# Kernel optimization log

Hardware: AMD Instinct MI355X
Metric: run time of the kernel (lower is better)

## Reference

```python
import jax, jax.numpy as jnp
import numpy as np

M_DIM = 1024
N_HEADS = 16
H_DIM = M_DIM // N_HEADS
FFN_H = 2 * M_DIM
B, S = 2, 2048
EPS = 1e-5
NEG = -1e9


def layernorm(x, g, b):
    mu = jnp.mean(x, axis=-1, keepdims=True)
    var = jnp.mean((x - mu) ** 2, axis=-1, keepdims=True)
    return (x - mu) * jax.lax.rsqrt(var + EPS) * g + b


def setup_inputs() -> dict:
    key = jax.random.key(0)
    ks = jax.random.split(key, 16)
    sc = 0.02
    return {
        "x": jax.random.normal(ks[0], (B, S, M_DIM), jnp.float32),
        "attention_mask": jnp.ones((B, S), jnp.int32),
        # per-head QKV projections stacked over heads: [H, M, D]
        "Wq": jax.random.normal(ks[1], (N_HEADS, M_DIM, H_DIM), jnp.float32) * sc,
        "bq": jnp.zeros((N_HEADS, H_DIM), jnp.float32),
        "Wk": jax.random.normal(ks[2], (N_HEADS, M_DIM, H_DIM), jnp.float32) * sc,
        "bk": jnp.zeros((N_HEADS, H_DIM), jnp.float32),
        "Wv": jax.random.normal(ks[3], (N_HEADS, M_DIM, H_DIM), jnp.float32) * sc,
        "bv": jnp.zeros((N_HEADS, H_DIM), jnp.float32),
        "Wo": jax.random.normal(ks[4], (M_DIM, M_DIM), jnp.float32) * sc,
        "bo": jnp.zeros((M_DIM,), jnp.float32),
        "g1": jnp.ones((M_DIM,), jnp.float32),
        "b1": jnp.zeros((M_DIM,), jnp.float32),
        "W1": jax.random.normal(ks[5], (M_DIM, FFN_H), jnp.float32) * sc,
        "bias1": jnp.zeros((FFN_H,), jnp.float32),
        "W2": jax.random.normal(ks[6], (FFN_H, M_DIM), jnp.float32) * sc,
        "bias2": jnp.zeros((M_DIM,), jnp.float32),
        "g2": jnp.ones((M_DIM,), jnp.float32),
        "b2": jnp.zeros((M_DIM,), jnp.float32),
    }


def reference(x, attention_mask, Wq, bq, Wk, bk, Wv, bv, Wo, bo, g1, b1, W1, bias1, W2, bias2, g2, b2):
    # All heads at once (the torch code loops over heads; same math).
    q = jnp.einsum("bsm,hmd->bhsd", x, Wq) + bq[None, :, None, :]
    k = jnp.einsum("bsm,hmd->bhsd", x, Wk) + bk[None, :, None, :]
    v = jnp.einsum("bsm,hmd->bhsd", x, Wv) + bv[None, :, None, :]
    scores = jnp.einsum("bhqd,bhkd->bhqk", q, k) / jnp.sqrt(jnp.float32(H_DIM))
    mask = attention_mask[:, None, None, :].astype(bool)  # [B,1,1,S] over keys
    scores = jnp.where(mask, scores, NEG)
    attn = jax.nn.softmax(scores, axis=-1)
    ctx = jnp.einsum("bhqk,bhkd->bhqd", attn, v)
    ctx = ctx.transpose(0, 2, 1, 3).reshape(x.shape[0], x.shape[1], M_DIM)  # concat heads
    out = ctx @ Wo + bo
    out = layernorm(out + x, g1, b1)
    fout = jax.nn.relu(out @ W1 + bias1) @ W2 + bias2
    out = layernorm(out + fout, g2, b2)
    return out
```

## Files before the change

### kernel.cpp

```cpp
#include <hip/hip_runtime.h>

#define MDIM 1024
#define FFH  2048
#define SEQ  2048
#define AST  72
#define VST  136
#define QSCL 0.18033688f

#if __has_builtin(__builtin_amdgcn_exp2f)
  #define EXP2(x) __builtin_amdgcn_exp2f(x)
#else
  #define EXP2(x) exp2f(x)
#endif

typedef __attribute__((ext_vector_type(8))) __bf16 bf16x8;
typedef __attribute__((ext_vector_type(4))) float floatx4;
typedef __attribute__((ext_vector_type(8))) unsigned short ushort8;
typedef __attribute__((address_space(3))) unsigned int lds_uint;
typedef const __attribute__((address_space(1))) unsigned int g_uint;

__device__ __forceinline__ unsigned short f2bf(float f){
  union { float f; unsigned u; } v; v.f = f;
  unsigned u = v.u;
  u += 0x7fffu + ((u >> 16) & 1u);
  return (unsigned short)(u >> 16);
}
__device__ __forceinline__ unsigned short f2bf_tr(float f){
  union { float f; unsigned u; } v; v.f = f;
  return (unsigned short)(v.u >> 16);
}

__global__ void k_cvt_qb(const float* __restrict__ x, unsigned short* __restrict__ xb,
                         const float* __restrict__ bq, const float* __restrict__ bk,
                         const float* __restrict__ bv, float* __restrict__ qbias){
  const int bid = blockIdx.x, t = threadIdx.x;
  if (bid < 4096){
    int i = (bid * 256 + t) * 4;
    float4 v = *(const float4*)(x + i);
    ushort4 o;
    o.x = f2bf(v.x); o.y = f2bf(v.y); o.z = f2bf(v.z); o.w = f2bf(v.w);
    *(ushort4*)(xb + i) = o;
  } else {
    int i = (bid - 4096) * 256 + t;
    qbias[i] = (i < 1024) ? bq[i] * QSCL : (i < 2048) ? bk[i - 1024] : bv[i - 2048];
  }
}

__global__ void __launch_bounds__(256) k_prep_w(const float* __restrict__ Wo, const float* __restrict__ W1,
                                                const float* __restrict__ W2, const float* __restrict__ Wq,
                                                const float* __restrict__ Wk, const float* __restrict__ Wv,
                                                unsigned short* __restrict__ wot, unsigned short* __restrict__ w1t,
                                                unsigned short* __restrict__ w2t, unsigned short* __restrict__ wqkvt){
  __shared__ unsigned short Ts[32 * 36];
  const int t = threadIdx.x, bid = blockIdx.x;
  const int lr = t >> 3, lc4 = (t & 7) << 2;
  if (bid >= 5120){
    const int id = bid - 5120;
    const int xm = id & 31, yd = (id >> 5) & 1, z = id >> 6;
    const int tensor = z >> 4, h = z & 15;
    const float* W = (tensor == 0) ? Wq : (tensor == 1) ? Wk : Wv;
    const float scl = (tensor == 0) ? QSCL : 1.0f;
    const int m0 = xm << 5, d0 = yd << 5;
    float4 v = *(const float4*)(W + ((size_t)h << 16) + (size_t)(m0 + lr) * 64 + d0 + lc4);
    ushort4 o; o.x = f2bf(v.x * scl); o.y = f2bf(v.y * scl); o.z = f2bf(v.z * scl); o.w = f2bf(v.w * scl);
    *(ushort4*)&Ts[lr * 36 + lc4] = o;
    __syncthreads();
    ushort4 w;
    w.x = Ts[(lc4 + 0) * 36 + lr];
    w.y = Ts[(lc4 + 1) * 36 + lr];
    w.z = Ts[(lc4 + 2) * 36 + lr];
    w.w = Ts[(lc4 + 3) * 36 + lr];
    const int n = (tensor << 10) + (h << 6) + d0 + lr;
    *(ushort4*)(wqkvt + ((size_t)n << 10) + m0 + lc4) = w;
    return;
  }
  const float* src; unsigned short* dst; int K, N, k0, n0;
  if (bid < 1024){
    src = Wo; dst = wot; K = 1024; N = 1024;
    n0 = (bid & 31) << 5; k0 = (bid >> 5) << 5;
  } else if (bid < 3072){
    const int id = bid - 1024;
    src = W1; dst = w1t; K = 1024; N = 2048;
    n0 = (id & 63) << 5; k0 = (id >> 6) << 5;
  } else {
    const int id = bid - 3072;
    src = W2; dst = w2t; K = 2048; N = 1024;
    n0 = (id & 31) << 5; k0 = (id >> 5) << 5;
  }
  float4 v = *(const float4*)(src + (size_t)(k0 + lr) * N + n0 + lc4);
  ushort4 o; o.x = f2bf(v.x); o.y = f2bf(v.y); o.z = f2bf(v.z); o.w = f2bf(v.w);
  *(ushort4*)&Ts[lr * 36 + lc4] = o;
  __syncthreads();
  ushort4 w;
  w.x = Ts[(lc4 + 0) * 36 + lr];
  w.y = Ts[(lc4 + 1) * 36 + lr];
  w.z = Ts[(lc4 + 2) * 36 + lr];
  w.w = Ts[(lc4 + 3) * 36 + lr];
  *(ushort4*)(dst + (size_t)(n0 + lr) * K + k0 + lc4) = w;
}

template<int RELU, int OUTBF>
__global__ void __launch_bounds__(256, 3) k_gemm128(const unsigned short* __restrict__ A,
                                                 const unsigned short* __restrict__ Bt,
                                                 const float* __restrict__ bias,
                                                 void* __restrict__ Cout, int N, int K){
  __shared__ unsigned short As[2][128 * 32];
  __shared__ unsigned short Bs[2][128 * 32];
  const int t = threadIdx.x;
  const int m0 = blockIdx.y << 7, n0 = blockIdx.x << 7;
  const int lane = t & 63, w = t >> 6;
  const int quad = lane >> 4, l16 = lane & 15;
  const int mw = (w & 1) << 6, nw = (w >> 1) << 6;
  floatx4 acc[4][4];
  #pragma unroll
  for (int i = 0; i < 4; i++)
    #pragma unroll
    for (int j = 0; j < 4; j++) acc[i][j] = (floatx4){0.f, 0.f, 0.f, 0.f};
  const unsigned short* Ag  = A  + (size_t)(m0 + (t >> 2)) * K + ((t & 3) << 3);
  const unsigned short* Ag2 = Ag + (size_t)64 * K;
  const unsigned short* Bg  = Bt + (size_t)(n0 + (t >> 2)) * K + ((t & 3) << 3);
  const unsigned short* Bg2 = Bg + (size_t)64 * K;

#define STG128(Ad, Bd, kb) { \
    __builtin_amdgcn_global_load_lds((g_uint*)(Ag  + (kb)), (lds_uint*)&(Ad)[t << 3],          16, 0, 0); \
    __builtin_amdgcn_global_load_lds((g_uint*)(Ag2 + (kb)), (lds_uint*)&(Ad)[(t << 3) + 2048], 16, 0, 0); \
    __builtin_amdgcn_global_load_lds((g_uint*)(Bg  + (kb)), (lds_uint*)&(Bd)[t << 3],          16, 0, 0); \
    __builtin_amdgcn_global_load_lds((g_uint*)(Bg2 + (kb)), (lds_uint*)&(Bd)[(t << 3) + 2048], 16, 0, 0); \
  }

  STG128(As[0], Bs[0], 0);
  __syncthreads();
  int cur = 0;
  for (int kb = 0; kb < K; kb += 32){
    if (kb + 32 < K) STG128(As[cur ^ 1], Bs[cur ^ 1], kb + 32);
    const unsigned short* Ar = As[cur];
    const unsigned short* Br = Bs[cur];
    bf16x8 af[4], bf[4];
    #pragma unroll
    for (int mt = 0; mt < 4; mt++)
      af[mt] = *(const bf16x8*)&Ar[((mw + (mt << 4) + l16) << 5) + (quad << 3)];
    #pragma unroll
    for (int nt = 0; nt < 4; nt++)
      bf[nt] = *(const bf16x8*)&Br[((nw + (nt << 4) + l16) << 5) + (quad << 3)];
    #pragma unroll
    for (int mt = 0; mt < 4; mt++)
      #pragma unroll
      for (int nt = 0; nt < 4; nt++)
        acc[mt][nt] = __builtin_amdgcn_mfma_f32_16x16x32_bf16(af[mt], bf[nt], acc[mt][nt], 0, 0, 0);
    __syncthreads();
    cur ^= 1;
  }
#undef STG128
  #pragma unroll
  for (int nt = 0; nt < 4; nt++){
    const int col = n0 + nw + (nt << 4) + l16;
    const float bsv = bias[col];
    #pragma unroll
    for (int mt = 0; mt < 4; mt++){
      const int row = m0 + mw + (mt << 4) + (quad << 2);
      #pragma unroll
      for (int r = 0; r < 4; r++){
        float v = acc[mt][nt][r] + bsv;
        if (RELU) v = fmaxf(v, 0.f);
        if (OUTBF) ((unsigned short*)Cout)[(size_t)(row + r) * N + col] = f2bf(v);
        else       ((float*)Cout)[(size_t)(row + r) * N + col] = v;
      }
    }
  }
}

template<int RELU, int OUTBF>
__global__ void __launch_bounds__(256) k_gemm64n(const unsigned short* __restrict__ A,
                                                 const unsigned short* __restrict__ Bt,
                                                 const float* __restrict__ bias,
                                                 void* __restrict__ Cout, int N, int K){
  __shared__ unsigned short As[2][2 * 128 * 32];
  __shared__ unsigned short Bs[2][2 * 64 * 32];
  const int t = threadIdx.x;
  const int m0 = blockIdx.y << 7, n0 = blockIdx.x << 6;
  const int lane = t & 63, w = t >> 6;
  const int quad = lane >> 4, l16 = lane & 15;
  const int mw = (w & 1) << 6, nw = (w >> 1) << 5;
  floatx4 acc[4][2];
  #pragma unroll
  for (int i = 0; i < 4; i++)
    #pragma unroll
    for (int j = 0; j < 2; j++) acc[i][j] = (floatx4){0.f, 0.f, 0.f, 0.f};
  const unsigned short* Ag  = A  + (size_t)(m0 + (t >> 2)) * K + ((t & 3) << 3);
  const unsigned short* Ag2 = Ag + (size_t)64 * K;
  const unsigned short* Bg  = Bt + (size_t)(n0 + (t >> 2)) * K + ((t & 3) << 3);

#define STG64(Ad, Bd, kb) { \
    _Pragma("unroll") \
    for (int s = 0; s < 2; s++){ \
      const int ko = (kb) + (s << 5); \
      __builtin_amdgcn_global_load_lds((g_uint*)(Ag  + ko), (lds_uint*)&(Ad)[(s << 12) + (t << 3)],        16, 0, 0); \
      __builtin_amdgcn_global_load_lds((g_uint*)(Ag2 + ko), (lds_uint*)&(Ad)[(s << 12) + (t << 3) + 2048], 16, 0, 0); \
      __builtin_amdgcn_global_load_lds((g_uint*)(Bg  + ko), (lds_uint*)&(Bd)[(s << 11) + (t << 3)],        16, 0, 0); \
    } }

  STG64(As[0], Bs[0], 0);
  __syncthreads();
  int cur = 0;
  for (int kb = 0; kb < K; kb += 64){
    if (kb + 64 < K) STG64(As[cur ^ 1], Bs[cur ^ 1], kb + 64);
    const unsigned short* Ar = As[cur];
    const unsigned short* Br = Bs[cur];
    #pragma unroll
    for (int s = 0; s < 2; s++){
      bf16x8 af[4], bf[2];
      #pragma unroll
      for (int mt = 0; mt < 4; mt++)
        af[mt] = *(const bf16x8*)&Ar[(s << 12) + ((mw + (mt << 4) + l16) << 5) + (quad << 3)];
      #pragma unroll
      for (int nt = 0; nt < 2; nt++)
        bf[nt] = *(const bf16x8*)&Br[(s << 11) + ((nw + (nt << 4) + l16) << 5) + (quad << 3)];
      #pragma unroll
      for (int mt = 0; mt < 4; mt++)
        #pragma unroll
        for (int nt = 0; nt < 2; nt++)
          acc[mt][nt] = __builtin_amdgcn_mfma_f32_16x16x32_bf16(af[mt], bf[nt], acc[mt][nt], 0, 0, 0);
    }
    __syncthreads();
    cur ^= 1;
  }
#undef STG64
  #pragma unroll
  for (int nt = 0; nt < 2; nt++){
    const int col = n0 + nw + (nt << 4) + l16;
    const float bsv = bias[col];
    #pragma unroll
    for (int mt = 0; mt < 4; mt++){
      const int row = m0 + mw + (mt << 4) + (quad << 2);
      #pragma unroll
      for (int r = 0; r < 4; r++){
        float v = acc[mt][nt][r] + bsv;
        if (RELU) v = fmaxf(v, 0.f);
        if (OUTBF) ((unsigned short*)Cout)[(size_t)(row + r) * N + col] = f2bf(v);
        else       ((float*)Cout)[(size_t)(row + r) * N + col] = v;
      }
    }
  }
}

__global__ void __launch_bounds__(256, 2) k_attn(const unsigned short* __restrict__ qkvb,
                                                 const int* __restrict__ amask,
                                                 unsigned short* __restrict__ ctxb){
  __shared__ __align__(16) unsigned short Ks[2][128 * AST];
  __shared__ __align__(16) unsigned short Vt[2][64 * VST];
  __shared__ __align__(16) int msk[2][128];
  const int t = threadIdx.x;
  const int w = t >> 6, lane = t & 63;
  const int quad = lane >> 4, l16 = lane & 15;
  const int lin = (blockIdx.y << 4) | blockIdx.x;
  const int xcd = lin & 7, jj = lin >> 3;
  const int bh = (xcd << 2) | (jj >> 4);
  const int b = bh >> 4, h = bh & 15;
  const int q0 = (jj & 15) << 7;
  const int r0 = (w << 5) + l16;
  const int r1 = r0 + 16;
  const int sr = t >> 2, sc = (t & 3) << 4;
  const int kg = t >> 4, dc = (t & 15) << 2;
  const int swz  = (dc >> 4) & 3;
  const int pc0  = ((((kg & 3) | ((kg >> 3) << 2)) ^ swz) << 3) | (((kg >> 2) & 1) << 2);

  {
    const int qr = t >> 1, qc = (t & 1) << 5;
    const unsigned short* qs = qkvb + (size_t)((b << 11) + q0 + qr) * 3072 + (h << 6) + qc;
    unsigned short* qd = &Ks[0][qr * AST + qc];
    *(uint4*)(qd)      = *(const uint4*)(qs);
    *(uint4*)(qd + 8)  = *(const uint4*)(qs + 8);
    *(uint4*)(qd + 16) = *(const uint4*)(qs + 16);
    *(uint4*)(qd + 24) = *(const uint4*)(qs + 24);
  }
  __syncthreads();
  const bf16x8 qa0 = *(const bf16x8*)&Ks[0][r0 * AST + (quad << 3)];
  const bf16x8 qa1 = *(const bf16x8*)&Ks[0][r0 * AST + (quad << 3) + 32];
  const bf16x8 qb0 = *(const bf16x8*)&Ks[0][r1 * AST + (quad << 3)];
  const bf16x8 qb1 = *(const bf16x8*)&Ks[0][r1 * AST + (quad << 3) + 32];

  floatx4 accA[4], accB[4];
  #pragma unroll
  for (int i = 0; i < 4; i++){
    accA[i] = (floatx4){0.f, 0.f, 0.f, 0.f};
    accB[i] = (floatx4){0.f, 0.f, 0.f, 0.f};
  }
  float l_runA = 0.f, l_runB = 0.f;

  const unsigned short* kbase  = qkvb + (size_t)((b << 11) + sr) * 3072 + 1024 + (h << 6) + sc;
  const unsigned short* kbase2 = kbase + (size_t)64 * 3072;
  const unsigned short* vbase  = qkvb + (size_t)((b << 11) + (kg << 2)) * 3072 + 2048 + (h << 6) + dc;
  const unsigned short* vbase2 = vbase + (size_t)64 * 3072;
  const int* mbase = amask + (b << 11);

  uint4 krA, krB, krC, krD;
  ushort4 va0, va1, va2, va3, vb0, vb1, vb2, vb3;
  int mreg = 1;

#define LOADT(tt) { \
    const size_t off = (size_t)((tt) << 7) * 3072; \
    krA = *(const uint4*)(kbase + off); \
    krB = *(const uint4*)(kbase + off + 8); \
    krC = *(const uint4*)(kbase2 + off); \
    krD = *(const uint4*)(kbase2 + off + 8); \
    va0 = *(const ushort4*)(vbase + off); \
    va1 = *(const ushort4*)(vbase + off + 3072); \
    va2 = *(const ushort4*)(vbase + off + 2 * 3072); \
    va3 = *(const ushort4*)(vbase + off + 3 * 3072); \
    vb0 = *(const ushort4*)(vbase2 + off); \
    vb1 = *(const ushort4*)(vbase2 + off + 3072); \
    vb2 = *(const ushort4*)(vbase2 + off + 2 * 3072); \
    vb3 = *(const ushort4*)(vbase2 + off + 3 * 3072); \
    if (t < 128) mreg = mbase[((tt) << 7) + t]; \
  }

#define STORET(dst) { \
    unsigned short* Kd = Ks[dst]; \
    unsigned short* Vd = Vt[dst]; \
    *(uint4*)&Kd[sr * AST + sc]            = krA; \
    *(uint4*)&Kd[sr * AST + sc + 8]        = krB; \
    *(uint4*)&Kd[(sr + 64) * AST + sc]     = krC; \
    *(uint4*)&Kd[(sr + 64) * AST + sc + 8] = krD; \
    ushort4 cc; \
    cc.x = va0.x; cc.y = va1.x; cc.z = va2.x; cc.w = va3.x; *(ushort4*)&Vd[(dc + 0) * VST + pc0] = cc; \
    cc.x = va0.y; cc.y = va1.y; cc.z = va2.y; cc.w = va3.y; *(ushort4*)&Vd[(dc + 1) * VST + pc0] = cc; \
    cc.x = va0.z; cc.y = va1.z; cc.z = va2.z; cc.w = va3.z; *(ushort4*)&Vd[(dc + 2) * VST + pc0] = cc; \
    cc.x = va0.w; cc.y = va1.w; cc.z = va2.w; cc.w = va3.w; *(ushort4*)&Vd[(dc + 3) * VST + pc0] = cc; \
    cc.x = vb0.x; cc.y = vb1.x; cc.z = vb2.x; cc.w = vb3.x; *(ushort4*)&Vd[(dc + 0) * VST + pc0 + 64] = cc; \
    cc.x = vb0.y; cc.y = vb1.y; cc.z = vb2.y; cc.w = vb3.y; *(ushort4*)&Vd[(dc + 1) * VST + pc0 + 64] = cc; \
    cc.x = vb0.z; cc.y = vb1.z; cc.z = vb2.z; cc.w = vb3.z; *(ushort4*)&Vd[(dc + 2) * VST + pc0 + 64] = cc; \
    cc.x = vb0.w; cc.y = vb1.w; cc.z = vb2.w; cc.w = vb3.w; *(ushort4*)&Vd[(dc + 3) * VST + pc0 + 64] = cc; \
    if (t < 128) msk[dst][t] = mreg; \
  }

  LOADT(0);
  __syncthreads();
  STORET(0);
  LOADT(1);
  __syncthreads();

  int c = 0;
  for (int kt = 0; kt < 16; kt++){
    if (kt + 1 < 16) STORET(c ^ 1);
    if (kt + 2 < 16) LOADT(kt + 2);
    {
      const unsigned short* Kc = Ks[c];
      const unsigned short* Vc = Vt[c];
      const int* Mc = msk[c];
      float lsA = 0.f, lsB = 0.f;
      #pragma unroll
      for (int s = 0; s < 4; s++){
        const unsigned short* kp = &Kc[((s << 5) + l16) * AST + (quad << 3)];
        const bf16x8 k00 = *(const bf16x8*)(kp);
        const bf16x8 k01 = *(const bf16x8*)(kp + 32);
        const bf16x8 k10 = *(const bf16x8*)(kp + (AST << 4));
        const bf16x8 k11 = *(const bf16x8*)(kp + (AST << 4) + 32);
        floatx4 sA0 = (floatx4){0.f, 0.f, 0.f, 0.f};
        floatx4 sB0 = (floatx4){0.f, 0.f, 0.f, 0.f};
        floatx4 sA1 = (floatx4){0.f, 0.f, 0.f, 0.f};
        floatx4 sB1 = (floatx4){0.f, 0.f, 0.f, 0.f};
        __builtin_amdgcn_s_setprio(1);
        sA0 = __builtin_amdgcn_mfma_f32_16x16x32_bf16(k00, qa0, sA0, 0, 0, 0);
        sA0 = __builtin_amdgcn_mfma_f32_16x16x32_bf16(k01, qa1, sA0, 0, 0, 0);
        sB0 = __builtin_amdgcn_mfma_f32_16x16x32_bf16(k00, qb0, sB0, 0, 0, 0);
        sB0 = __builtin_amdgcn_mfma_f32_16x16x32_bf16(k01, qb1, sB0, 0, 0, 0);
        sA1 = __builtin_amdgcn_mfma_f32_16x16x32_bf16(k10, qa0, sA1, 0, 0, 0);
        sA1 = __builtin_amdgcn_mfma_f32_16x16x32_bf16(k11, qa1, sA1, 0, 0, 0);
        sB1 = __builtin_amdgcn_mfma_f32_16x16x32_bf16(k10, qb0, sB1, 0, 0, 0);
        sB1 = __builtin_amdgcn_mfma_f32_16x16x32_bf16(k11, qb1, sB1, 0, 0, 0);
        __builtin_amdgcn_s_setprio(0);
        const int4 m0 = *(const int4*)&Mc[(s << 5) + (quad << 2)];
        const int4 m1 = *(const int4*)&Mc[(s << 5) + 16 + (quad << 2)];
        const float a0 = m0.x ? EXP2(sA0[0]) : 0.f;
        const float a1 = m0.y ? EXP2(sA0[1]) : 0.f;
        const float a2 = m0.z ? EXP2(sA0[2]) : 0.f;
        const float a3 = m0.w ? EXP2(sA0[3]) : 0.f;
        const float a4 = m1.x ? EXP2(sA1[0]) : 0.f;
        const float a5 = m1.y ? EXP2(sA1[1]) : 0.f;
        const float a6 = m1.z ? EXP2(sA1[2]) : 0.f;
        const float a7 = m1.w ? EXP2(sA1[3]) : 0.f;
        const float b0 = m0.x ? EXP2(sB0[0]) : 0.f;
        const float b1 = m0.y ? EXP2(sB0[1]) : 0.f;
        const float b2 = m0.z ? EXP2(sB0[2]) : 0.f;
        const float b3 = m0.w ? EXP2(sB0[3]) : 0.f;
        const float b4 = m1.x ? EXP2(sB1[0]) : 0.f;
        const float b5 = m1.y ? EXP2(sB1[1]) : 0.f;
        const float b6 = m1.z ? EXP2(sB1[2]) : 0.f;
        const float b7 = m1.w ? EXP2(sB1[3]) : 0.f;
        lsA += (a0 + a1) + (a2 + a3) + (a4 + a5) + (a6 + a7);
        lsB += (b0 + b1) + (b2 + b3) + (b4 + b5) + (b6 + b7);
        ushort8 uA, uB;
        uA[0] = f2bf_tr(a0); uA[1] = f2bf_tr(a1); uA[2] = f2bf_tr(a2); uA[3] = f2bf_tr(a3);
        uA[4] = f2bf_tr(a4); uA[5] = f2bf_tr(a5); uA[6] = f2bf_tr(a6); uA[7] = f2bf_tr(a7);
        uB[0] = f2bf_tr(b0); uB[1] = f2bf_tr(b1); uB[2] = f2bf_tr(b2); uB[3] = f2bf_tr(b3);
        uB[4] = f2bf_tr(b4); uB[5] = f2bf_tr(b5); uB[6] = f2bf_tr(b6); uB[7] = f2bf_tr(b7);
        const bf16x8 pfA = __builtin_bit_cast(bf16x8, uA);
        const bf16x8 pfB = __builtin_bit_cast(bf16x8, uB);
        __builtin_amdgcn_s_setprio(1);
        #pragma unroll
        for (int mt = 0; mt < 4; mt++){
          const bf16x8 vf = *(const bf16x8*)&Vc[((mt << 4) + l16) * VST + ((((s << 2) + quad) ^ mt) << 3)];
          accA[mt] = __builtin_amdgcn_mfma_f32_16x16x32_bf16(vf, pfA, accA[mt], 0, 0, 0);
          accB[mt] = __builtin_amdgcn_mfma_f32_16x16x32_bf16(vf, pfB, accB[mt], 0, 0, 0);
        }
        __builtin_amdgcn_s_setprio(0);
      }
      l_runA += lsA;
      l_runB += lsB;
    }
    __syncthreads();
    c ^= 1;
  }
#undef LOADT
#undef STORET

  l_runA += __shfl_xor(l_runA, 16);
  l_runA += __shfl_xor(l_runA, 32);
  l_runB += __shfl_xor(l_runB, 16);
  l_runB += __shfl_xor(l_runB, 32);
  const float liA = 1.f / l_runA;
  const float liB = 1.f / l_runB;
  unsigned short* oA = ctxb + (size_t)((b << 11) + q0 + r0) * 1024 + (h << 6);
  unsigned short* oB = ctxb + (size_t)((b << 11) + q0 + r1) * 1024 + (h << 6);
  #pragma unroll
  for (int mt = 0; mt < 4; mt++){
    ushort4 o;
    o.x = f2bf(accA[mt][0] * liA);
    o.y = f2bf(accA[mt][1] * liA);
    o.z = f2bf(accA[mt][2] * liA);
    o.w = f2bf(accA[mt][3] * liA);
    *(ushort4*)&oA[(mt << 4) + (quad << 2)] = o;
    o.x = f2bf(accB[mt][0] * liB);
    o.y = f2bf(accB[mt][1] * liB);
    o.z = f2bf(accB[mt][2] * liB);
    o.w = f2bf(accB[mt][3] * liB);
    *(ushort4*)&oB[(mt << 4) + (quad << 2)] = o;
  }
}

__global__ void __launch_bounds__(256) k_ln(const unsigned short* __restrict__ a,
                                            const float* __restrict__ res,
                                            const float* __restrict__ gg, const float* __restrict__ bb,
                                            float* __restrict__ out, unsigned short* __restrict__ outb){
  const int row = blockIdx.x, t = threadIdx.x;
  const ushort4 au = ((const ushort4*)(a + (size_t)row * 1024))[t];
  const float4 rv = ((const float4*)(res + (size_t)row * 1024))[t];
  float4 v;
  { union { unsigned u; float f; } c;
    c.u = (unsigned)au.x << 16; v.x = c.f + rv.x;
    c.u = (unsigned)au.y << 16; v.y = c.f + rv.y;
    c.u = (unsigned)au.z << 16; v.z = c.f + rv.z;
    c.u = (unsigned)au.w << 16; v.w = c.f + rv.w; }
  float sum = v.x + v.y + v.z + v.w;
  float ss  = v.x * v.x + v.y * v.y + v.z * v.z + v.w * v.w;
  #pragma unroll
  for (int off = 32; off > 0; off >>= 1){
    sum += __shfl_down(sum, off);
    ss  += __shfl_down(ss, off);
  }
  __shared__ float red[8];
  const int w = t >> 6;
  if ((t & 63) == 0){ red[w] = sum; red[4 + w] = ss; }
  __syncthreads();
  const float S  = red[0] + red[1] + red[2] + red[3];
  const float SS = red[4] + red[5] + red[6] + red[7];
  const float mu  = S * (1.f / 1024.f);
  const float var = SS * (1.f / 1024.f) - mu * mu;
  const float rs  = rsqrtf(var + 1e-5f);
  const float4 gv = ((const float4*)gg)[t];
  const float4 bv = ((const float4*)bb)[t];
  float4 o;
  o.x = (v.x - mu) * rs * gv.x + bv.x;
  o.y = (v.y - mu) * rs * gv.y + bv.y;
  o.z = (v.z - mu) * rs * gv.z + bv.z;
  o.w = (v.w - mu) * rs * gv.w + bv.w;
  ((float4*)(out + (size_t)row * 1024))[t] = o;
  if (outb){
    ushort4 ob; ob.x = f2bf(o.x); ob.y = f2bf(o.y); ob.z = f2bf(o.z); ob.w = f2bf(o.w);
    ((ushort4*)(outb + (size_t)row * 1024))[t] = ob;
  }
}

extern "C" void kernel_launch(void* const* d_in, const int* in_sizes, int n_in,
                              void* d_out, int out_size, void* d_ws, size_t ws_size,
                              hipStream_t stream){
  const float* x     = (const float*)d_in[0];
  const int*   amask = (const int*)d_in[1];
  const float* Wq    = (const float*)d_in[2];
  const float* bq    = (const float*)d_in[3];
  const float* Wk    = (const float*)d_in[4];
  const float* bk    = (const float*)d_in[5];
  const float* Wv    = (const float*)d_in[6];
  const float* bv    = (const float*)d_in[7];
  const float* Wo    = (const float*)d_in[8];
  const float* bo    = (const float*)d_in[9];
  const float* g1    = (const float*)d_in[10];
  const float* b1    = (const float*)d_in[11];
  const float* W1    = (const float*)d_in[12];
  const float* bias1 = (const float*)d_in[13];
  const float* W2    = (const float*)d_in[14];
  const float* bias2 = (const float*)d_in[15];
  const float* g2    = (const float*)d_in[16];
  const float* b2    = (const float*)d_in[17];

  char* ws = (char*)d_ws;
  unsigned short* xb    = (unsigned short*)(ws + 0);
  unsigned short* wqkvt = (unsigned short*)(ws + 8388608);
  float*          qbias = (float*)         (ws + 14680064);
  unsigned short* wot   = (unsigned short*)(ws + 14692352);
  unsigned short* w1t   = (unsigned short*)(ws + 16789504);
  unsigned short* w2t   = (unsigned short*)(ws + 20983808);
  unsigned short* ctxb  = (unsigned short*)(ws + 25178112);
  unsigned short* attnb = (unsigned short*)(ws + 33566720);
  unsigned short* fbufb = attnb;
  unsigned short* qkvb  = (unsigned short*)(ws + 50343936);
  float*          out1  = (float*)         (ws + 50343936);
  unsigned short* out1b = (unsigned short*)(ws + 50343936 + 25165824);
  unsigned short* h1    = (unsigned short*)(ws + 50343936 + 33554432);

  k_cvt_qb<<<dim3(4108), dim3(256), 0, stream>>>(x, xb, bq, bk, bv, qbias);
  k_prep_w<<<dim3(8192), dim3(256), 0, stream>>>(Wo, W1, W2, Wq, Wk, Wv, wot, w1t, w2t, wqkvt);

  k_gemm128<0,1><<<dim3(24, 32), dim3(256), 0, stream>>>(xb, wqkvt, qbias, qkvb, 3072, 1024);
  k_attn<<<dim3(16, 32), dim3(256), 0, stream>>>(qkvb, amask, ctxb);
  k_gemm64n<0,1><<<dim3(16, 32), dim3(256), 0, stream>>>(ctxb, wot, bo, attnb, MDIM, 1024);
  k_ln<<<dim3(4096), dim3(256), 0, stream>>>(attnb, x, g1, b1, out1, out1b);
  k_gemm128<1,1><<<dim3(16, 32), dim3(256), 0, stream>>>(out1b, w1t, bias1, h1, FFH, 1024);
  k_gemm64n<0,1><<<dim3(16, 32), dim3(256), 0, stream>>>(h1, w2t, bias2, fbufb, MDIM, 2048);
  k_ln<<<dim3(4096), dim3(256), 0, stream>>>(fbufb, out1, g2, b2, (float*)d_out, nullptr);
}
```

Measured before the change: 297.2 us.

## Software-pipeline QK MFMAs one sub-tile ahead of softmax/PV in attention

Splits each 32-key sub-step of the attention inner loop into a QK^T MFMA stage and an exp/convert/PV stage, then interleaves them so the QK scores for sub-tile s+1 are issued before finishing sub-tile s. The aim is to hide MFMA latency behind the exp and conversion VALU work. It also drops the XCD-aware block index remapping in favour of a direct blockIdx mapping, which changes how heads spread over L2 domains. The extra live score registers may raise register pressure, which matters under launch_bounds(256,2).

```diff
diff --git a/kernel.cpp b/kernel.cpp
--- a/kernel.cpp
+++ b/kernel.cpp
@@ -252,11 +252,8 @@
   const int t = threadIdx.x;
   const int w = t >> 6, lane = t & 63;
   const int quad = lane >> 4, l16 = lane & 15;
-  const int lin = (blockIdx.y << 4) | blockIdx.x;
-  const int xcd = lin & 7, jj = lin >> 3;
-  const int bh = (xcd << 2) | (jj >> 4);
-  const int b = bh >> 4, h = bh & 15;
-  const int q0 = (jj & 15) << 7;
+  const int b = blockIdx.y >> 4, h = blockIdx.y & 15;
+  const int q0 = blockIdx.x << 7;
   const int r0 = (w << 5) + l16;
   const int r1 = r0 + 16;
   const int sr = t >> 2, sc = (t & 3) << 4;
@@ -333,6 +330,66 @@
     if (t < 128) msk[dst][t] = mreg; \
   }
 
+#define QKISS(s, SA0, SB0, SA1, SB1) { \
+    const unsigned short* kp = &Kc[(((s) << 5) + l16) * AST + (quad << 3)]; \
+    const bf16x8 k00 = *(const bf16x8*)(kp); \
+    const bf16x8 k01 = *(const bf16x8*)(kp + 32); \
+    const bf16x8 k10 = *(const bf16x8*)(kp + (AST << 4)); \
+    const bf16x8 k11 = *(const bf16x8*)(kp + (AST << 4) + 32); \
+    SA0 = (floatx4){0.f, 0.f, 0.f, 0.f}; \
+    SB0 = (floatx4){0.f, 0.f, 0.f, 0.f}; \
+    SA1 = (floatx4){0.f, 0.f, 0.f, 0.f}; \
+    SB1 = (floatx4){0.f, 0.f, 0.f, 0.f}; \
+    __builtin_amdgcn_s_setprio(1); \
+    SA0 = __builtin_amdgcn_mfma_f32_16x16x32_bf16(k00, qa0, SA0, 0, 0, 0); \
+    SA0 = __builtin_amdgcn_mfma_f32_16x16x32_bf16(k01, qa1, SA0, 0, 0, 0); \
+    SB0 = __builtin_amdgcn_mfma_f32_16x16x32_bf16(k00, qb0, SB0, 0, 0, 0); \
+    SB0 = __builtin_amdgcn_mfma_f32_16x16x32_bf16(k01, qb1, SB0, 0, 0, 0); \
+    SA1 = __builtin_amdgcn_mfma_f32_16x16x32_bf16(k10, qa0, SA1, 0, 0, 0); \
+    SA1 = __builtin_amdgcn_mfma_f32_16x16x32_bf16(k11, qa1, SA1, 0, 0, 0); \
+    SB1 = __builtin_amdgcn_mfma_f32_16x16x32_bf16(k10, qb0, SB1, 0, 0, 0); \
+    SB1 = __builtin_amdgcn_mfma_f32_16x16x32_bf16(k11, qb1, SB1, 0, 0, 0); \
+    __builtin_amdgcn_s_setprio(0); \
+  }
+
+#define FIN(s, SA0, SB0, SA1, SB1) { \
+    const int4 m0 = *(const int4*)&Mc[((s) << 5) + (quad << 2)]; \
+    const int4 m1 = *(const int4*)&Mc[((s) << 5) + 16 + (quad << 2)]; \
+    const float a0 = m0.x ? EXP2(SA0[0]) : 0.f; \
+    const float a1 = m0.y ? EXP2(SA0[1]) : 0.f; \
+    const float a2 = m0.z ? EXP2(SA0[2]) : 0.f; \
+    const float a3 = m0.w ? EXP2(SA0[3]) : 0.f; \
+    const float a4 = m1.x ? EXP2(SA1[0]) : 0.f; \
+    const float a5 = m1.y ? EXP2(SA1[1]) : 0.f; \
+    const float a6 = m1.z ? EXP2(SA1[2]) : 0.f; \
+    const float a7 = m1.w ? EXP2(SA1[3]) : 0.f; \
+    const float b0 = m0.x ? EXP2(SB0[0]) : 0.f; \
+    const float b1 = m0.y ? EXP2(SB0[1]) : 0.f; \
+    const float b2 = m0.z ? EXP2(SB0[2]) : 0.f; \
+    const float b3 = m0.w ? EXP2(SB0[3]) : 0.f; \
+    const float b4 = m1.x ? EXP2(SB1[0]) : 0.f; \
+    const float b5 = m1.y ? EXP2(SB1[1]) : 0.f; \
+    const float b6 = m1.z ? EXP2(SB1[2]) : 0.f; \
+    const float b7 = m1.w ? EXP2(SB1[3]) : 0.f; \
+    lsA += (a0 + a1) + (a2 + a3) + (a4 + a5) + (a6 + a7); \
+    lsB += (b0 + b1) + (b2 + b3) + (b4 + b5) + (b6 + b7); \
+    ushort8 uA, uB; \
+    uA[0] = f2bf_tr(a0); uA[1] = f2bf_tr(a1); uA[2] = f2bf_tr(a2); uA[3] = f2bf_tr(a3); \
+    uA[4] = f2bf_tr(a4); uA[5] = f2bf_tr(a5); uA[6] = f2bf_tr(a6); uA[7] = f2bf_tr(a7); \
+    uB[0] = f2bf_tr(b0); uB[1] = f2bf_tr(b1); uB[2] = f2bf_tr(b2); uB[3] = f2bf_tr(b3); \
+    uB[4] = f2bf_tr(b4); uB[5] = f2bf_tr(b5); uB[6] = f2bf_tr(b6); uB[7] = f2bf_tr(b7); \
+    const bf16x8 pfA = __builtin_bit_cast(bf16x8, uA); \
+    const bf16x8 pfB = __builtin_bit_cast(bf16x8, uB); \
+    __builtin_amdgcn_s_setprio(1); \
+    _Pragma("unroll") \
+    for (int mt = 0; mt < 4; mt++){ \
+      const bf16x8 vf = *(const bf16x8*)&Vc[((mt << 4) + l16) * VST + (((((s) << 2) + quad) ^ mt) << 3)]; \
+      accA[mt] = __builtin_amdgcn_mfma_f32_16x16x32_bf16(vf, pfA, accA[mt], 0, 0, 0); \
+      accB[mt] = __builtin_amdgcn_mfma_f32_16x16x32_bf16(vf, pfB, accB[mt], 0, 0, 0); \
+    } \
+    __builtin_amdgcn_s_setprio(0); \
+  }
+
   LOADT(0);
   __syncthreads();
   STORET(0);
@@ -348,63 +405,16 @@
       const unsigned short* Vc = Vt[c];
       const int* Mc = msk[c];
       float lsA = 0.f, lsB = 0.f;
-      #pragma unroll
-      for (int s = 0; s < 4; s++){
-        const unsigned short* kp = &Kc[((s << 5) + l16) * AST + (quad << 3)];
-        const bf16x8 k00 = *(const bf16x8*)(kp);
-        const bf16x8 k01 = *(const bf16x8*)(kp + 32);
-        const bf16x8 k10 = *(const bf16x8*)(kp + (AST << 4));
-        const bf16x8 k11 = *(const bf16x8*)(kp + (AST << 4) + 32);
-        floatx4 sA0 = (floatx4){0.f, 0.f, 0.f, 0.f};
-        floatx4 sB0 = (floatx4){0.f, 0.f, 0.f, 0.f};
-        floatx4 sA1 = (floatx4){0.f, 0.f, 0.f, 0.f};
-        floatx4 sB1 = (floatx4){0.f, 0.f, 0.f, 0.f};
-        __builtin_amdgcn_s_setprio(1);
-        sA0 = __builtin_amdgcn_mfma_f32_16x16x32_bf16(k00, qa0, sA0, 0, 0, 0);
-        sA0 = __builtin_amdgcn_mfma_f32_16x16x32_bf16(k01, qa1, sA0, 0, 0, 0);
-        sB0 = __builtin_amdgcn_mfma_f32_16x16x32_bf16(k00, qb0, sB0, 0, 0, 0);
-        sB0 = __builtin_amdgcn_mfma_f32_16x16x32_bf16(k01, qb1, sB0, 0, 0, 0);
-        sA1 = __builtin_amdgcn_mfma_f32_16x16x32_bf16(k10, qa0, sA1, 0, 0, 0);
-        sA1 = __builtin_amdgcn_mfma_f32_16x16x32_bf16(k11, qa1, sA1, 0, 0, 0);
-        sB1 = __builtin_amdgcn_mfma_f32_16x16x32_bf16(k10, qb0, sB1, 0, 0, 0);
-        sB1 = __builtin_amdgcn_mfma_f32_16x16x32_bf16(k11, qb1, sB1, 0, 0, 0);
-        __builtin_amdgcn_s_setprio(0);
-        const int4 m0 = *(const int4*)&Mc[(s << 5) + (quad << 2)];
-        const int4 m1 = *(const int4*)&Mc[(s << 5) + 16 + (quad << 2)];
-        const float a0 = m0.x ? EXP2(sA0[0]) : 0.f;
-        const float a1 = m0.y ? EXP2(sA0[1]) : 0.f;
-        const float a2 = m0.z ? EXP2(sA0[2]) : 0.f;
-        const float a3 = m0.w ? EXP2(sA0[3]) : 0.f;
-        const float a4 = m1.x ? EXP2(sA1[0]) : 0.f;
-        const float a5 = m1.y ? EXP2(sA1[1]) : 0.f;
-        const float a6 = m1.z ? EXP2(sA1[2]) : 0.f;
-        const float a7 = m1.w ? EXP2(sA1[3]) : 0.f;
-        const float b0 = m0.x ? EXP2(sB0[0]) : 0.f;
-        const float b1 = m0.y ? EXP2(sB0[1]) : 0.f;
-        const float b2 = m0.z ? EXP2(sB0[2]) : 0.f;
-        const float b3 = m0.w ? EXP2(sB0[3]) : 0.f;
-        const float b4 = m1.x ? EXP2(sB1[0]) : 0.f;
-        const float b5 = m1.y ? EXP2(sB1[1]) : 0.f;
-        const float b6 = m1.z ? EXP2(sB1[2]) : 0.f;
-        const float b7 = m1.w ? EXP2(sB1[3]) : 0.f;
-        lsA += (a0 + a1) + (a2 + a3) + (a4 + a5) + (a6 + a7);
-        lsB += (b0 + b1) + (b2 + b3) + (b4 + b5) + (b6 + b7);
-        ushort8 uA, uB;
-        uA[0] = f2bf_tr(a0); uA[1] = f2bf_tr(a1); uA[2] = f2bf_tr(a2); uA[3] = f2bf_tr(a3);
-        uA[4] = f2bf_tr(a4); uA[5] = f2bf_tr(a5); uA[6] = f2bf_tr(a6); uA[7] = f2bf_tr(a7);
-        uB[0] = f2bf_tr(b0); uB[1] = f2bf_tr(b1); uB[2] = f2bf_tr(b2); uB[3] = f2bf_tr(b3);
-        uB[4] = f2bf_tr(b4); uB[5] = f2bf_tr(b5); uB[6] = f2bf_tr(b6); uB[7] = f2bf_tr(b7);
-        const bf16x8 pfA = __builtin_bit_cast(bf16x8, uA);
-        const bf16x8 pfB = __builtin_bit_cast(bf16x8, uB);
-        __builtin_amdgcn_s_setprio(1);
-        #pragma unroll
-        for (int mt = 0; mt < 4; mt++){
-          const bf16x8 vf = *(const bf16x8*)&Vc[((mt << 4) + l16) * VST + ((((s << 2) + quad) ^ mt) << 3)];
-          accA[mt] = __builtin_amdgcn_mfma_f32_16x16x32_bf16(vf, pfA, accA[mt], 0, 0, 0);
-          accB[mt] = __builtin_amdgcn_mfma_f32_16x16x32_bf16(vf, pfB, accB[mt], 0, 0, 0);
-        }
-        __builtin_amdgcn_s_setprio(0);
-      }
+      floatx4 xA0, xB0, xA1, xB1;
+      floatx4 yA0, yB0, yA1, yB1;
+      QKISS(0, xA0, xB0, xA1, xB1);
+      QKISS(1, yA0, yB0, yA1, yB1);
+      FIN  (0, xA0, xB0, xA1, xB1);
+      QKISS(2, xA0, xB0, xA1, xB1);
+      FIN  (1, yA0, yB0, yA1, yB1);
+      QKISS(3, yA0, yB0, yA1, yB1);
+      FIN  (2, xA0, xB0, xA1, xB1);
+      FIN  (3, yA0, yB0, yA1, yB1);
       l_runA += lsA;
       l_runB += lsB;
     }
@@ -413,6 +423,8 @@
   }
 #undef LOADT
 #undef STORET
+#undef QKISS
+#undef FIN
 
   l_runA += __shfl_xor(l_runA, 16);
   l_runA += __shfl_xor(l_runA, 32);
```

New measurement: 302.2 us. No clear change (+1.7%).

## Single-buffer attention K/V tiles in LDS and raise occupancy to four blocks

Applied to the files above, without the earlier changes.

The attention kernel drops the double-buffered K/V/mask LDS tiles for a single buffer. Each iteration now stores the register-prefetched tile, syncs, then prefetches the next tile into registers while computing. Launch bounds go from 2 to 4 blocks per CU, and the XCD-aware block-index remapping is replaced by a plain blockIdx mapping. The aim is more resident waves to hide latency, at the cost of an extra barrier per tile, less LDS-level overlap, tighter register limits and possibly worse L2 locality across XCDs.

```diff
diff --git a/kernel.cpp b/kernel.cpp
--- a/kernel.cpp
+++ b/kernel.cpp
@@ -243,20 +243,17 @@
   }
 }
 
-__global__ void __launch_bounds__(256, 2) k_attn(const unsigned short* __restrict__ qkvb,
+__global__ void __launch_bounds__(256, 4) k_attn(const unsigned short* __restrict__ qkvb,
                                                  const int* __restrict__ amask,
                                                  unsigned short* __restrict__ ctxb){
-  __shared__ __align__(16) unsigned short Ks[2][128 * AST];
-  __shared__ __align__(16) unsigned short Vt[2][64 * VST];
-  __shared__ __align__(16) int msk[2][128];
+  __shared__ __align__(16) unsigned short Ks[128 * AST];
+  __shared__ __align__(16) unsigned short Vt[64 * VST];
+  __shared__ __align__(16) int msk[128];
   const int t = threadIdx.x;
   const int w = t >> 6, lane = t & 63;
   const int quad = lane >> 4, l16 = lane & 15;
-  const int lin = (blockIdx.y << 4) | blockIdx.x;
-  const int xcd = lin & 7, jj = lin >> 3;
-  const int bh = (xcd << 2) | (jj >> 4);
-  const int b = bh >> 4, h = bh & 15;
-  const int q0 = (jj & 15) << 7;
+  const int b = blockIdx.y >> 4, h = blockIdx.y & 15;
+  const int q0 = blockIdx.x << 7;
   const int r0 = (w << 5) + l16;
   const int r1 = r0 + 16;
   const int sr = t >> 2, sc = (t & 3) << 4;
@@ -267,17 +264,17 @@
   {
     const int qr = t >> 1, qc = (t & 1) << 5;
     const unsigned short* qs = qkvb + (size_t)((b << 11) + q0 + qr) * 3072 + (h << 6) + qc;
-    unsigned short* qd = &Ks[0][qr * AST + qc];
+    unsigned short* qd = &Ks[qr * AST + qc];
     *(uint4*)(qd)      = *(const uint4*)(qs);
     *(uint4*)(qd + 8)  = *(const uint4*)(qs + 8);
     *(uint4*)(qd + 16) = *(const uint4*)(qs + 16);
     *(uint4*)(qd + 24) = *(const uint4*)(qs + 24);
   }
   __syncthreads();
-  const bf16x8 qa0 = *(const bf16x8*)&Ks[0][r0 * AST + (quad << 3)];
-  const bf16x8 qa1 = *(const bf16x8*)&Ks[0][r0 * AST + (quad << 3) + 32];
-  const bf16x8 qb0 = *(const bf16x8*)&Ks[0][r1 * AST + (quad << 3)];
-  const bf16x8 qb1 = *(const bf16x8*)&Ks[0][r1 * AST + (quad << 3) + 32];
+  const bf16x8 qa0 = *(const bf16x8*)&Ks[r0 * AST + (quad << 3)];
+  const bf16x8 qa1 = *(const bf16x8*)&Ks[r0 * AST + (quad << 3) + 32];
+  const bf16x8 qb0 = *(const bf16x8*)&Ks[r1 * AST + (quad << 3)];
+  const bf16x8 qb1 = *(const bf16x8*)&Ks[r1 * AST + (quad << 3) + 32];
 
   floatx4 accA[4], accB[4];
   #pragma unroll
@@ -314,43 +311,35 @@
     if (t < 128) mreg = mbase[((tt) << 7) + t]; \
   }
 
-#define STORET(dst) { \
-    unsigned short* Kd = Ks[dst]; \
-    unsigned short* Vd = Vt[dst]; \
-    *(uint4*)&Kd[sr * AST + sc]            = krA; \
-    *(uint4*)&Kd[sr * AST + sc + 8]        = krB; \
-    *(uint4*)&Kd[(sr + 64) * AST + sc]     = krC; \
-    *(uint4*)&Kd[(sr + 64) * AST + sc + 8] = krD; \
+#define STORET() { \
+    *(uint4*)&Ks[sr * AST + sc]            = krA; \
+    *(uint4*)&Ks[sr * AST + sc + 8]        = krB; \
+    *(uint4*)&Ks[(sr + 64) * AST + sc]     = krC; \
+    *(uint4*)&Ks[(sr + 64) * AST + sc + 8] = krD; \
     ushort4 cc; \
-    cc.x = va0.x; cc.y = va1.x; cc.z = va2.x; cc.w = va3.x; *(ushort4*)&Vd[(dc + 0) * VST + pc0] = cc; \
-    cc.x = va0.y; cc.y = va1.y; cc.z = va2.y; cc.w = va3.y; *(ushort4*)&Vd[(dc + 1) * VST + pc0] = cc; \
-    cc.x = va0.z; cc.y = va1.z; cc.z = va2.z; cc.w = va3.z; *(ushort4*)&Vd[(dc + 2) * VST + pc0] = cc; \
-    cc.x = va0.w; cc.y = va1.w; cc.z = va2.w; cc.w = va3.w; *(ushort4*)&Vd[(dc + 3) * VST + pc0] = cc; \
-    cc.x = vb0.x; cc.y = vb1.x; cc.z = vb2.x; cc.w = vb3.x; *(ushort4*)&Vd[(dc + 0) * VST + pc0 + 64] = cc; \
-    cc.x = vb0.y; cc.y = vb1.y; cc.z = vb2.y; cc.w = vb3.y; *(ushort4*)&Vd[(dc + 1) * VST + pc0 + 64] = cc; \
-    cc.x = vb0.z; cc.y = vb1.z; cc.z = vb2.z; cc.w = vb3.z; *(ushort4*)&Vd[(dc + 2) * VST + pc0 + 64] = cc; \
-    cc.x = vb0.w; cc.y = vb1.w; cc.z = vb2.w; cc.w = vb3.w; *(ushort4*)&Vd[(dc + 3) * VST + pc0 + 64] = cc; \
-    if (t < 128) msk[dst][t] = mreg; \
+    cc.x = va0.x; cc.y = va1.x; cc.z = va2.x; cc.w = va3.x; *(ushort4*)&Vt[(dc + 0) * VST + pc0] = cc; \
+    cc.x = va0.y; cc.y = va1.y; cc.z = va2.y; cc.w = va3.y; *(ushort4*)&Vt[(dc + 1) * VST + pc0] = cc; \
+    cc.x = va0.z; cc.y = va1.z; cc.z = va2.z; cc.w = va3.z; *(ushort4*)&Vt[(dc + 2) * VST + pc0] = cc; \
+    cc.x = va0.w; cc.y = va1.w; cc.z = va2.w; cc.w = va3.w; *(ushort4*)&Vt[(dc + 3) * VST + pc0] = cc; \
+    cc.x = vb0.x; cc.y = vb1.x; cc.z = vb2.x; cc.w = vb3.x; *(ushort4*)&Vt[(dc + 0) * VST + pc0 + 64] = cc; \
+    cc.x = vb0.y; cc.y = vb1.y; cc.z = vb2.y; cc.w = vb3.y; *(ushort4*)&Vt[(dc + 1) * VST + pc0 + 64] = cc; \
+    cc.x = vb0.z; cc.y = vb1.z; cc.z = vb2.z; cc.w = vb3.z; *(ushort4*)&Vt[(dc + 2) * VST + pc0 + 64] = cc; \
+    cc.x = vb0.w; cc.y = vb1.w; cc.z = vb2.w; cc.w = vb3.w; *(ushort4*)&Vt[(dc + 3) * VST + pc0 + 64] = cc; \
+    if (t < 128) msk[t] = mreg; \
   }
 
   LOADT(0);
   __syncthreads();
-  STORET(0);
-  LOADT(1);
-  __syncthreads();
-
-  int c = 0;
+
   for (int kt = 0; kt < 16; kt++){
-    if (kt + 1 < 16) STORET(c ^ 1);
-    if (kt + 2 < 16) LOADT(kt + 2);
+    STORET();
+    __syncthreads();
+    if (kt + 1 < 16) LOADT(kt + 1);
     {
-      const unsigned short* Kc = Ks[c];
-      const unsigned short* Vc = Vt[c];
-      const int* Mc = msk[c];
       float lsA = 0.f, lsB = 0.f;
       #pragma unroll
       for (int s = 0; s < 4; s++){
-        const unsigned short* kp = &Kc[((s << 5) + l16) * AST + (quad << 3)];
+        const unsigned short* kp = &Ks[((s << 5) + l16) * AST + (quad << 3)];
         const bf16x8 k00 = *(const bf16x8*)(kp);
         const bf16x8 k01 = *(const bf16x8*)(kp + 32);
         const bf16x8 k10 = *(const bf16x8*)(kp + (AST << 4));
@@ -369,8 +358,8 @@
         sB1 = __builtin_amdgcn_mfma_f32_16x16x32_bf16(k10, qb0, sB1, 0, 0, 0);
         sB1 = __builtin_amdgcn_mfma_f32_16x16x32_bf16(k11, qb1, sB1, 0, 0, 0);
         __builtin_amdgcn_s_setprio(0);
-        const int4 m0 = *(const int4*)&Mc[(s << 5) + (quad << 2)];
-        const int4 m1 = *(const int4*)&Mc[(s << 5) + 16 + (quad << 2)];
+        const int4 m0 = *(const int4*)&msk[(s << 5) + (quad << 2)];
+        const int4 m1 = *(const int4*)&msk[(s << 5) + 16 + (quad << 2)];
         const float a0 = m0.x ? EXP2(sA0[0]) : 0.f;
         const float a1 = m0.y ? EXP2(sA0[1]) : 0.f;
         const float a2 = m0.z ? EXP2(sA0[2]) : 0.f;
@@ -399,7 +388,7 @@
         __builtin_amdgcn_s_setprio(1);
         #pragma unroll
         for (int mt = 0; mt < 4; mt++){
-          const bf16x8 vf = *(const bf16x8*)&Vc[((mt << 4) + l16) * VST + ((((s << 2) + quad) ^ mt) << 3)];
+          const bf16x8 vf = *(const bf16x8*)&Vt[((mt << 4) + l16) * VST + ((((s << 2) + quad) ^ mt) << 3)];
           accA[mt] = __builtin_amdgcn_mfma_f32_16x16x32_bf16(vf, pfA, accA[mt], 0, 0, 0);
           accB[mt] = __builtin_amdgcn_mfma_f32_16x16x32_bf16(vf, pfB, accB[mt], 0, 0, 0);
         }
@@ -409,7 +398,6 @@
       l_runB += lsB;
     }
     __syncthreads();
-    c ^= 1;
   }
 #undef LOADT
 #undef STORET
```

After: 437.7 us. 1.47x slower.
